# Performance work log

Hardware: AMD Instinct MI355X
Metric: run time of the kernel (lower is better)

Reference implementation:

```python
import jax, jax.numpy as jnp
import numpy as np

# Dimensions chosen per init_kwargs / input_specs
B, INC, OUTC, H, W = 16, 512, 256, 32, 32
FD = H * W           # flattened_dim = 1024 (perfect square)
DK = INC // 4        # 128, projection dim of the rotatory attention
EPS_BN = 1e-5


def setup_inputs() -> dict:
    key = jax.random.key(0)
    ks = jax.random.split(key, 8)
    sc = lambda fan_in: 1.0 / np.sqrt(fan_in)
    return {
        "x": jax.random.normal(ks[0], (B, INC, H, W), jnp.float32),
        "s": jax.random.normal(ks[1], (B, OUTC, 2 * H, 2 * W), jnp.float32),
        # ConvTranspose2d(inc, outc, 2, 2): torch weight shape (in, out, kH, kW)
        "up_w": jax.random.normal(ks[2], (INC, OUTC, 2, 2), jnp.float32) * sc(INC * 4),
        "up_b": jnp.zeros((OUTC,), jnp.float32),
        # LinearRotatoryAttentionModule projections: Linear(flattened_dim, inc//4) x3
        "wq": jax.random.normal(ks[3], (FD, DK), jnp.float32) * sc(FD),
        "wkl": jax.random.normal(ks[4], (FD, DK), jnp.float32) * sc(FD),
        "wkr": jax.random.normal(ks[5], (FD, DK), jnp.float32) * sc(FD),
        # conv_block(2*outc, outc): Conv2d 3x3 pad 1 + BatchNorm + ReLU
        "c1_w": jax.random.normal(ks[6], (OUTC, 2 * OUTC, 3, 3), jnp.float32) * sc(2 * OUTC * 9),
        "c1_b": jnp.zeros((OUTC,), jnp.float32),
        "bn_g": jnp.ones((OUTC,), jnp.float32),
        "bn_b": jnp.zeros((OUTC,), jnp.float32),
    }


def _rotatory(l, x, r, wq, wkl, wkr):
    """Linear rotatory attention on one triplet of slices, each (INC, FD).
    Center queries left and right contexts via elu+1 linear attention."""
    phi = lambda t: jax.nn.elu(t) + 1.0
    q = phi(x @ wq)        # (N, Dk)
    kl = phi(l @ wkl)      # (N, Dk)
    kr = phi(r @ wkr)      # (N, Dk)

    def linattn(k, v):
        kv = jnp.einsum('nk,nd->kd', k, v)      # (Dk, D)
        z = q @ k.sum(0) + 1e-6                  # (N,)
        return (q @ kv) / z[:, None]             # (N, D)

    return x + linattn(kl, l) + linattn(kr, r)


def reference(x, s, up_w, up_b, wq, wkl, wkr, c1_w, c1_b, bn_g, bn_b):
    # --- rotatory attention over interior batch samples (vectorized, no Python loop) ---
    xf = x.reshape(B, INC, FD)
    mid = jax.vmap(_rotatory, in_axes=(0, 0, 0, None, None, None))(
        xf[:-2], xf[1:-1], xf[2:], wq, wkl, wkr)          # (B-2, INC, FD)
    new = jnp.concatenate([x[:1], mid.reshape(B - 2, INC, H, W), x[-1:]], axis=0)

    # --- ConvTranspose2d k=2 s=2: non-overlapping, exact as einsum + reshape ---
    up = jnp.einsum('ncij,coab->noiajb', new, up_w).reshape(B, OUTC, 2 * H, 2 * W)
    up = up + up_b[None, :, None, None]

    # --- fused gate: sigmoid(relu(up + s)), then channel concat with skip ---
    g = jax.nn.sigmoid(jax.nn.relu(up + s))
    cat = jnp.concatenate([g, s], axis=1)                  # (B, 2*OUTC, 2H, 2W)

    # --- conv_block: Conv 3x3 same + BatchNorm (batch stats) + ReLU ---
    y = jax.lax.conv_general_dilated(cat, c1_w, (1, 1), 'SAME',
                                     dimension_numbers=('NCHW', 'OIHW', 'NCHW'))
    y = y + c1_b[None, :, None, None]
    mu = y.mean(axis=(0, 2, 3), keepdims=True)
    var = y.var(axis=(0, 2, 3), keepdims=True)
    y = (y - mu) / jnp.sqrt(var + EPS_BN)
    y = y * bn_g[None, :, None, None] + bn_b[None, :, None, None]
    return jax.nn.relu(y)
```

## Files before the change

### kernel.cpp

```cpp
#include <hip/hip_runtime.h>
#include <math.h>

#define B_ 16
#define INC 512
#define OUTC 256
#define FD 1024
#define DK 128
#define T_ 14
#define HO 64
#define WO 64
#define SP (HO*WO)
#define KCP 40

typedef unsigned short u16;
typedef __attribute__((ext_vector_type(8))) short shortx8;
typedef __attribute__((ext_vector_type(4))) float floatx4;

__device__ __forceinline__ float phi_f(float t) {
    return t > 0.0f ? t + 1.0f : expf(t);
}
__device__ __forceinline__ u16 f2bf(float f) {
    unsigned int u = __float_as_uint(f);
    unsigned int r = (u + 0x7fffu + ((u >> 16) & 1u)) >> 16;
    return (u16)r;
}
__device__ __forceinline__ float bf2f(u16 h) {
    return __uint_as_float(((unsigned int)h) << 16);
}

__global__ __launch_bounds__(256) void kprep_x(const float* __restrict__ x, u16* __restrict__ xT) {
    __shared__ u16 T[64][65];
    int d0 = blockIdx.x * 64, c0 = blockIdx.y * 64, b = blockIdx.z;
    const float* src = x + (size_t)b * INC * FD;
    int tid = threadIdx.x, lr = tid >> 6, lc = tid & 63;
    #pragma unroll
    for (int i = 0; i < 16; ++i) {
        int c = lr + i * 4;
        T[lc][c] = f2bf(src[(size_t)(c0 + c) * FD + d0 + lc]);
    }
    __syncthreads();
    u16* dst = xT + (size_t)b * FD * INC;
    #pragma unroll
    for (int i = 0; i < 16; ++i) {
        int d = lr + i * 4;
        dst[(size_t)(d0 + d) * INC + c0 + lc] = T[d][lc];
    }
}

__global__ __launch_bounds__(256) void ktr_w(const float* __restrict__ src, u16* __restrict__ dst,
                                             int R, int C) {
    __shared__ u16 T[64][65];
    int c0 = blockIdx.x * 64, r0 = blockIdx.y * 64;
    int tid = threadIdx.x, lr = tid >> 6, lc = tid & 63;
    #pragma unroll
    for (int i = 0; i < 16; ++i) {
        int r = lr + i * 4;
        T[lc][r] = f2bf(src[(size_t)(r0 + r) * C + c0 + lc]);
    }
    __syncthreads();
    #pragma unroll
    for (int i = 0; i < 16; ++i) {
        int c = lr + i * 4;
        dst[(size_t)(c0 + c) * R + r0 + lc] = T[c][lc];
    }
}

__global__ void kw_tr(const float* __restrict__ c1_w, u16* __restrict__ Wt) {
    int i = blockIdx.x * 256 + threadIdx.x;
    if (i >= 256 * 512 * 9) return;
    int tap = i % 9; int t2 = i / 9;
    int c = t2 % 512; int o = t2 / 512;
    Wt[((size_t)tap * 256 + o) * 512 + c] = f2bf(c1_w[i]);
}

__global__ __launch_bounds__(256) void k1_proj(const float* __restrict__ x,
        const u16* __restrict__ wqT, const u16* __restrict__ wklT, const u16* __restrict__ wkrT,
        u16* __restrict__ qb, u16* __restrict__ klt, u16* __restrict__ krt) {
    __shared__ u16 smem[8704];
    u16* As = smem;
    u16* Bs = smem + 5120;
    int z = blockIdx.z, t = z / 3, which = z - t * 3;
    int src = (which == 0) ? t + 1 : (which == 1 ? t : t + 2);
    const float* Af = x + (size_t)src * INC * FD;
    const u16* Bw = (which == 0) ? wqT : (which == 1 ? wklT : wkrT);
    int n0 = blockIdx.x * 64, m0 = blockIdx.y * 128;
    int tid = threadIdx.x, w = tid >> 6, lane = tid & 63, l15 = lane & 15, quad = lane >> 4;
    int sm = tid >> 2, sq = (tid & 3) * 8;
    floatx4 acc[2][4];
    #pragma unroll
    for (int i = 0; i < 2; ++i)
        #pragma unroll
        for (int j = 0; j < 4; ++j) acc[i][j] = (floatx4){0.f,0.f,0.f,0.f};

    for (int k0 = 0; k0 < FD; k0 += 32) {
        float4 v0 = *(const float4*)&Af[(size_t)(m0 + sm) * FD + k0 + sq];
        float4 v1 = *(const float4*)&Af[(size_t)(m0 + sm) * FD + k0 + sq + 4];
        float4 v2 = *(const float4*)&Af[(size_t)(m0 + 64 + sm) * FD + k0 + sq];
        float4 v3 = *(const float4*)&Af[(size_t)(m0 + 64 + sm) * FD + k0 + sq + 4];
        union { u16 h[8]; uint4 v; } p0, p1;
        p0.h[0]=f2bf(v0.x); p0.h[1]=f2bf(v0.y); p0.h[2]=f2bf(v0.z); p0.h[3]=f2bf(v0.w);
        p0.h[4]=f2bf(v1.x); p0.h[5]=f2bf(v1.y); p0.h[6]=f2bf(v1.z); p0.h[7]=f2bf(v1.w);
        p1.h[0]=f2bf(v2.x); p1.h[1]=f2bf(v2.y); p1.h[2]=f2bf(v2.z); p1.h[3]=f2bf(v2.w);
        p1.h[4]=f2bf(v3.x); p1.h[5]=f2bf(v3.y); p1.h[6]=f2bf(v3.z); p1.h[7]=f2bf(v3.w);
        *(uint4*)&As[sm * 40 + sq] = p0.v;
        *(uint4*)&As[(64 + sm) * 40 + sq] = p1.v;
        *(uint4*)&Bs[sm * 40 + sq] = *(const uint4*)&Bw[(size_t)(n0 + sm) * FD + k0 + sq];
        __syncthreads();
        shortx8 bfr[4];
        #pragma unroll
        for (int nt = 0; nt < 4; ++nt)
            bfr[nt] = *(const shortx8*)&Bs[(nt * 16 + l15) * 40 + quad * 8];
        #pragma unroll
        for (int mt = 0; mt < 2; ++mt) {
            shortx8 af = *(const shortx8*)&As[(w * 32 + mt * 16 + l15) * 40 + quad * 8];
            #pragma unroll
            for (int nt = 0; nt < 4; ++nt)
                acc[mt][nt] = __builtin_amdgcn_mfma_f32_16x16x32_bf16(af, bfr[nt], acc[mt][nt], 0, 0, 0);
        }
        __syncthreads();
    }
    if (which == 0) {
        u16* outp = qb + (size_t)t * INC * DK;
        #pragma unroll
        for (int mt = 0; mt < 2; ++mt)
            #pragma unroll
            for (int nt = 0; nt < 4; ++nt)
                #pragma unroll
                for (int r = 0; r < 4; ++r) {
                    int m_out = m0 + w * 32 + mt * 16 + quad * 4 + r;
                    int n_out = n0 + nt * 16 + l15;
                    outp[(size_t)m_out * DK + n_out] = f2bf(phi_f(acc[mt][nt][r]));
                }
    } else {
        u16* outp = ((which == 1) ? klt : krt) + (size_t)t * DK * INC;
        #pragma unroll
        for (int mt = 0; mt < 2; ++mt)
            #pragma unroll
            for (int nt = 0; nt < 4; ++nt)
                #pragma unroll
                for (int r = 0; r < 4; ++r) {
                    int mloc = w * 32 + mt * 16 + quad * 4 + r;
                    int nloc = nt * 16 + l15;
                    smem[nloc * 136 + mloc] = f2bf(phi_f(acc[mt][nt][r]));
                }
        __syncthreads();
        int dkl = tid >> 2, seg = tid & 3;
        const uint4* sp = (const uint4*)&smem[dkl * 136 + seg * 32];
        uint4* dp = (uint4*)&outp[(size_t)(n0 + dkl) * INC + m0 + seg * 32];
        dp[0] = sp[0]; dp[1] = sp[1]; dp[2] = sp[2]; dp[3] = sp[3];
    }
}

__global__ void k2b_ksum(const u16* __restrict__ klt, const u16* __restrict__ krt,
                         float* __restrict__ ksuml, float* __restrict__ ksumr) {
    int t = blockIdx.x; int dk = threadIdx.x;
    const u16* pl = klt + ((size_t)t * DK + dk) * INC;
    const u16* pr = krt + ((size_t)t * DK + dk) * INC;
    float s1 = 0.f, s2 = 0.f;
    for (int n = 0; n < INC; ++n) { s1 += bf2f(pl[n]); s2 += bf2f(pr[n]); }
    ksuml[t * DK + dk] = s1; ksumr[t * DK + dk] = s2;
}

__global__ void k2c_z(const u16* __restrict__ qb, const float* __restrict__ ksuml,
                      const float* __restrict__ ksumr, float* __restrict__ zl, float* __restrict__ zr) {
    int t = blockIdx.x; int n = threadIdx.x;
    const u16* q = qb + ((size_t)t * INC + n) * DK;
    const float* sl = ksuml + t * DK;
    const float* sr = ksumr + t * DK;
    float a = 0.f, b = 0.f;
    for (int k = 0; k < DK; ++k) { float qv = bf2f(q[k]); a = fmaf(qv, sl[k], a); b = fmaf(qv, sr[k], b); }
    zl[t * INC + n] = a + 1e-6f;
    zr[t * INC + n] = b + 1e-6f;
}

__global__ __launch_bounds__(256) void k2_kv(const u16* __restrict__ xT,
        const u16* __restrict__ klt, const u16* __restrict__ krt,
        u16* __restrict__ kvlT, u16* __restrict__ kvrT) {
    __shared__ u16 As[128 * 40];
    __shared__ u16 Bs[64 * 40];
    int z = blockIdx.z, t = z >> 1, side = z & 1;
    const u16* A = xT + (size_t)(side ? t + 2 : t) * FD * INC;
    const u16* Bw = (side ? krt : klt) + (size_t)t * DK * INC;
    u16* outp = (side ? kvrT : kvlT) + (size_t)t * FD * DK;
    int n0 = blockIdx.x * 64, m0 = blockIdx.y * 128;
    int tid = threadIdx.x, w = tid >> 6, lane = tid & 63, l15 = lane & 15, quad = lane >> 4;
    int sm = tid >> 2, sq = (tid & 3) * 8;
    floatx4 acc[2][4];
    #pragma unroll
    for (int i = 0; i < 2; ++i)
        #pragma unroll
        for (int j = 0; j < 4; ++j) acc[i][j] = (floatx4){0.f,0.f,0.f,0.f};
    for (int k0 = 0; k0 < INC; k0 += 32) {
        *(uint4*)&As[sm * 40 + sq] = *(const uint4*)&A[(size_t)(m0 + sm) * INC + k0 + sq];
        *(uint4*)&As[(64 + sm) * 40 + sq] = *(const uint4*)&A[(size_t)(m0 + 64 + sm) * INC + k0 + sq];
        *(uint4*)&Bs[sm * 40 + sq] = *(const uint4*)&Bw[(size_t)(n0 + sm) * INC + k0 + sq];
        __syncthreads();
        shortx8 bfr[4];
        #pragma unroll
        for (int nt = 0; nt < 4; ++nt)
            bfr[nt] = *(const shortx8*)&Bs[(nt * 16 + l15) * 40 + quad * 8];
        #pragma unroll
        for (int mt = 0; mt < 2; ++mt) {
            shortx8 af = *(const shortx8*)&As[(w * 32 + mt * 16 + l15) * 40 + quad * 8];
            #pragma unroll
            for (int nt = 0; nt < 4; ++nt)
                acc[mt][nt] = __builtin_amdgcn_mfma_f32_16x16x32_bf16(af, bfr[nt], acc[mt][nt], 0, 0, 0);
        }
        __syncthreads();
    }
    #pragma unroll
    for (int mt = 0; mt < 2; ++mt)
        #pragma unroll
        for (int nt = 0; nt < 4; ++nt)
            #pragma unroll
            for (int r = 0; r < 4; ++r) {
                int m_out = m0 + w * 32 + mt * 16 + quad * 4 + r;
                int n_out = n0 + nt * 16 + l15;
                outp[(size_t)m_out * DK + n_out] = f2bf(acc[mt][nt][r]);
            }
}

__global__ __launch_bounds__(256) void k3_out(const u16* __restrict__ xT,
        const u16* __restrict__ qb, const u16* __restrict__ kvlT, const u16* __restrict__ kvrT,
        const float* __restrict__ zl, const float* __restrict__ zr, u16* __restrict__ newT) {
    __shared__ u16 As1[128 * 40];
    __shared__ u16 As2[128 * 40];
    __shared__ u16 Bs[64 * 40];
    int t = blockIdx.z;
    const u16* A1 = kvlT + (size_t)t * FD * DK;
    const u16* A2 = kvrT + (size_t)t * FD * DK;
    const u16* Bq = qb + (size_t)t * INC * DK;
    int n0 = blockIdx.x * 64, m0 = blockIdx.y * 128;
    int tid = threadIdx.x, w = tid >> 6, lane = tid & 63, l15 = lane & 15, quad = lane >> 4;
    int sm = tid >> 2, sq = (tid & 3) * 8;
    floatx4 accl[2][4], accr[2][4];
    #pragma unroll
    for (int i = 0; i < 2; ++i)
        #pragma unroll
        for (int j = 0; j < 4; ++j) {
            accl[i][j] = (floatx4){0.f,0.f,0.f,0.f};
            accr[i][j] = (floatx4){0.f,0.f,0.f,0.f};
        }
    for (int k0 = 0; k0 < DK; k0 += 32) {
        *(uint4*)&As1[sm * 40 + sq] = *(const uint4*)&A1[(size_t)(m0 + sm) * DK + k0 + sq];
        *(uint4*)&As1[(64 + sm) * 40 + sq] = *(const uint4*)&A1[(size_t)(m0 + 64 + sm) * DK + k0 + sq];
        *(uint4*)&As2[sm * 40 + sq] = *(const uint4*)&A2[(size_t)(m0 + sm) * DK + k0 + sq];
        *(uint4*)&As2[(64 + sm) * 40 + sq] = *(const uint4*)&A2[(size_t)(m0 + 64 + sm) * DK + k0 + sq];
        *(uint4*)&Bs[sm * 40 + sq] = *(const uint4*)&Bq[(size_t)(n0 + sm) * DK + k0 + sq];
        __syncthreads();
        shortx8 bfr[4];
        #pragma unroll
        for (int nt = 0; nt < 4; ++nt)
            bfr[nt] = *(const shortx8*)&Bs[(nt * 16 + l15) * 40 + quad * 8];
        #pragma unroll
        for (int mt = 0; mt < 2; ++mt) {
            shortx8 afl = *(const shortx8*)&As1[(w * 32 + mt * 16 + l15) * 40 + quad * 8];
            shortx8 afr = *(const shortx8*)&As2[(w * 32 + mt * 16 + l15) * 40 + quad * 8];
            #pragma unroll
            for (int nt = 0; nt < 4; ++nt) {
                accl[mt][nt] = __builtin_amdgcn_mfma_f32_16x16x32_bf16(afl, bfr[nt], accl[mt][nt], 0, 0, 0);
                accr[mt][nt] = __builtin_amdgcn_mfma_f32_16x16x32_bf16(afr, bfr[nt], accr[mt][nt], 0, 0, 0);
            }
        }
        __syncthreads();
    }
    float il[4], ir[4];
    #pragma unroll
    for (int nt = 0; nt < 4; ++nt) {
        int n_out = n0 + nt * 16 + l15;
        il[nt] = 1.0f / zl[t * INC + n_out];
        ir[nt] = 1.0f / zr[t * INC + n_out];
    }
    const u16* xc = xT + (size_t)(t + 1) * FD * INC;
    u16* outp = newT + (size_t)t * FD * INC;
    #pragma unroll
    for (int mt = 0; mt < 2; ++mt)
        #pragma unroll
        for (int nt = 0; nt < 4; ++nt)
            #pragma unroll
            for (int r = 0; r < 4; ++r) {
                int m_out = m0 + w * 32 + mt * 16 + quad * 4 + r;
                int n_out = n0 + nt * 16 + l15;
                float xv = bf2f(xc[(size_t)m_out * INC + n_out]);
                float v = xv + accl[mt][nt][r] * il[nt] + accr[mt][nt][r] * ir[nt];
                outp[(size_t)m_out * INC + n_out] = f2bf(v);
            }
}

__global__ __launch_bounds__(256) void k4_up(const u16* __restrict__ xT,
        const u16* __restrict__ newT, const u16* __restrict__ upwT,
        const float* __restrict__ up_b, u16* __restrict__ P) {
    __shared__ u16 As[128 * 40];
    __shared__ u16 Bs[64 * 40];
    int b = blockIdx.z;
    const u16* A = (b == 0) ? xT
                 : (b == B_ - 1) ? (xT + (size_t)(B_ - 1) * FD * INC)
                 : (newT + (size_t)(b - 1) * FD * INC);
    int n0 = blockIdx.x * 64, m0 = blockIdx.y * 128;
    int tid = threadIdx.x, w = tid >> 6, lane = tid & 63, l15 = lane & 15, quad = lane >> 4;
    int sm = tid >> 2, sq = (tid & 3) * 8;
    floatx4 acc[2][4];
    #pragma unroll
    for (int i = 0; i < 2; ++i)
        #pragma unroll
        for (int j = 0; j < 4; ++j) acc[i][j] = (floatx4){0.f,0.f,0.f,0.f};
    for (int k0 = 0; k0 < INC; k0 += 32) {
        *(uint4*)&As[sm * 40 + sq] = *(const uint4*)&A[(size_t)(m0 + sm) * INC + k0 + sq];
        *(uint4*)&As[(64 + sm) * 40 + sq] = *(const uint4*)&A[(size_t)(m0 + 64 + sm) * INC + k0 + sq];
        *(uint4*)&Bs[sm * 40 + sq] = *(const uint4*)&upwT[(size_t)(n0 + sm) * INC + k0 + sq];
        __syncthreads();
        shortx8 bfr[4];
        #pragma unroll
        for (int nt = 0; nt < 4; ++nt)
            bfr[nt] = *(const shortx8*)&Bs[(nt * 16 + l15) * 40 + quad * 8];
        #pragma unroll
        for (int mt = 0; mt < 2; ++mt) {
            shortx8 af = *(const shortx8*)&As[(w * 32 + mt * 16 + l15) * 40 + quad * 8];
            #pragma unroll
            for (int nt = 0; nt < 4; ++nt)
                acc[mt][nt] = __builtin_amdgcn_mfma_f32_16x16x32_bf16(af, bfr[nt], acc[mt][nt], 0, 0, 0);
        }
        __syncthreads();
    }
    #pragma unroll
    for (int mt = 0; mt < 2; ++mt)
        #pragma unroll
        for (int nt = 0; nt < 4; ++nt) {
            int mm = n0 + nt * 16 + l15;
            int o = mm >> 2, aa = (mm >> 1) & 1, cb = mm & 1;
            float bias = up_b[o];
            #pragma unroll
            for (int r = 0; r < 4; ++r) {
                int px = m0 + w * 32 + mt * 16 + quad * 4 + r;
                int ii = px >> 5, jj = px & 31;
                int p = 2 * ii + aa, q = 2 * jj + cb;
                size_t pos = ((size_t)(b * 66 + 1 + p) * 66 + 1 + q) * 512;
                float sv = bf2f(P[pos + 256 + o]);
                float up = acc[mt][nt][r] + bias;
                float rr = fmaxf(up + sv, 0.0f);
                P[pos + o] = f2bf(1.0f / (1.0f + expf(-rr)));
            }
        }
}

__global__ __launch_bounds__(256) void k4b_sfill(const float* __restrict__ s_in,
                                                 u16* __restrict__ P) {
    __shared__ u16 T[64 * 264];
    int p = blockIdx.x;
    int b = blockIdx.y;
    int tid = threadIdx.x;
    int qcol = tid & 63;
    int ob = tid >> 6;
    for (int o = ob; o < 256; o += 4) {
        float v = s_in[((size_t)(b * OUTC + o) * HO + p) * WO + qcol];
        T[qcol * 264 + o] = f2bf(v);
    }
    __syncthreads();
    int q2 = tid >> 2;
    int sg = tid & 3;
    size_t base = ((size_t)(b * 66 + 1 + p) * 66 + 1 + q2) * 512 + 256;
    #pragma unroll
    for (int it = 0; it < 8; ++it) {
        int seg = sg + it * 4;
        uint4 v = *(const uint4*)&T[q2 * 264 + seg * 8];
        *(uint4*)(P + base + seg * 8) = v;
    }
}

__global__ __launch_bounds__(256) void k5_mfma(const u16* __restrict__ P,
        const u16* __restrict__ Wt, const float* __restrict__ c1_b,
        float* __restrict__ y) {
    __shared__ u16 Xs[6 * 66 * KCP];
    int rb = blockIdx.x;
    int o0 = blockIdx.y * 64;
    int b  = blockIdx.z;
    int tid = threadIdx.x;
    int w = tid >> 6, lane = tid & 63;
    int l15 = lane & 15, quad = lane >> 4;

    floatx4 acc[4][4];
    #pragma unroll
    for (int i = 0; i < 4; ++i)
        #pragma unroll
        for (int j = 0; j < 4; ++j)
            acc[i][j] = (floatx4){0.f, 0.f, 0.f, 0.f};

    size_t Pbase = ((size_t)b * 66 + (size_t)rb * 4) * 66 * 512;

    for (int ch = 0; ch < 16; ++ch) {
        int c0 = ch * 32;
        __syncthreads();
        for (int s = tid; s < 1584; s += 256) {
            int r = s / 264; int rem = s - r * 264;
            int col = rem >> 2; int cs = rem & 3;
            uint4 v = *(const uint4*)(P + Pbase + ((size_t)r * 66 + col) * 512 + c0 + cs * 8);
            *(uint4*)&Xs[(r * 66 + col) * KCP + cs * 8] = v;
        }
        __syncthreads();
        #pragma unroll
        for (int dy = 0; dy < 3; ++dy) {
            #pragma unroll
            for (int dx = 0; dx < 3; ++dx) {
                int tap = dy * 3 + dx;
                shortx8 wf[4];
                #pragma unroll
                for (int nt = 0; nt < 4; ++nt)
                    wf[nt] = *(const shortx8*)(Wt +
                        ((size_t)(tap * 256 + o0 + nt * 16 + l15)) * 512 + c0 + quad * 8);
                #pragma unroll
                for (int mt = 0; mt < 4; ++mt) {
                    shortx8 af = *(const shortx8*)&Xs[((w + dy) * 66 + mt * 16 + l15 + dx) * KCP + quad * 8];
                    #pragma unroll
                    for (int nt = 0; nt < 4; ++nt)
                        acc[mt][nt] = __builtin_amdgcn_mfma_f32_16x16x32_bf16(
                            af, wf[nt], acc[mt][nt], 0, 0, 0);
                }
            }
        }
    }
    int row = rb * 4 + w;
    float bias[4];
    #pragma unroll
    for (int nt = 0; nt < 4; ++nt) bias[nt] = c1_b[o0 + nt * 16 + l15];
    #pragma unroll
    for (int mt = 0; mt < 4; ++mt) {
        #pragma unroll
        for (int nt = 0; nt < 4; ++nt) {
            int o = o0 + nt * 16 + l15;
            size_t ybase = (size_t)(b * OUTC + o) * SP + row * 64;
            #pragma unroll
            for (int r = 0; r < 4; ++r) {
                int col = mt * 16 + quad * 4 + r;
                y[ybase + col] = acc[mt][nt][r] + bias[nt];
            }
        }
    }
}

__global__ __launch_bounds__(256) void k6_bnred(const float* __restrict__ y,
        float* __restrict__ bnsum, float* __restrict__ bnsq) {
    int b = blockIdx.x, o = blockIdx.y;
    const float* p = y + ((size_t)b * OUTC + o) * SP;
    float s1 = 0.f, s2 = 0.f;
    for (int i = threadIdx.x; i < SP; i += 256) { float v = p[i]; s1 += v; s2 = fmaf(v, v, s2); }
    #pragma unroll
    for (int off = 32; off > 0; off >>= 1) {
        s1 += __shfl_down(s1, off, 64);
        s2 += __shfl_down(s2, off, 64);
    }
    __shared__ float r1[4], r2[4];
    int wid = threadIdx.x >> 6, lane = threadIdx.x & 63;
    if (lane == 0) { r1[wid] = s1; r2[wid] = s2; }
    __syncthreads();
    if (threadIdx.x == 0) {
        atomicAdd(&bnsum[o], r1[0] + r1[1] + r1[2] + r1[3]);
        atomicAdd(&bnsq[o],  r2[0] + r2[1] + r2[2] + r2[3]);
    }
}

__global__ void k7_bnfin(const float* __restrict__ bnsum, const float* __restrict__ bnsq,
                         const float* __restrict__ bn_g, const float* __restrict__ bn_b,
                         float* __restrict__ scale, float* __restrict__ shift) {
    int o = threadIdx.x;
    float cnt = (float)(B_ * SP);
    float mu = bnsum[o] / cnt;
    float var = bnsq[o] / cnt - mu * mu;
    float sc = bn_g[o] * rsqrtf(var + 1e-5f);
    scale[o] = sc;
    shift[o] = bn_b[o] - mu * sc;
}

__global__ __launch_bounds__(256) void k8_apply(float* __restrict__ y,
        const float* __restrict__ scale, const float* __restrict__ shift) {
    int i = blockIdx.x * 256 + threadIdx.x;
    int o = (i >> 10) & 255;
    float4 v = ((float4*)y)[i];
    float sc = scale[o], sh = shift[o];
    v.x = fmaxf(fmaf(v.x, sc, sh), 0.f);
    v.y = fmaxf(fmaf(v.y, sc, sh), 0.f);
    v.z = fmaxf(fmaf(v.z, sc, sh), 0.f);
    v.w = fmaxf(fmaf(v.w, sc, sh), 0.f);
    ((float4*)y)[i] = v;
}

extern "C" void kernel_launch(void* const* d_in, const int* in_sizes, int n_in,
                              void* d_out, int out_size, void* d_ws, size_t ws_size,
                              hipStream_t stream) {
    const float* x    = (const float*)d_in[0];
    const float* s_in = (const float*)d_in[1];
    const float* up_w = (const float*)d_in[2];
    const float* up_b = (const float*)d_in[3];
    const float* wq   = (const float*)d_in[4];
    const float* wkl  = (const float*)d_in[5];
    const float* wkr  = (const float*)d_in[6];
    const float* c1_w = (const float*)d_in[7];
    const float* c1_b = (const float*)d_in[8];
    const float* bn_g = (const float*)d_in[9];
    const float* bn_b = (const float*)d_in[10];
    float* y = (float*)d_out;
    float* ws = (float*)d_ws;

    size_t off = 0;
    float* ksuml = ws + off; off += (size_t)T_ * DK;
    float* ksumr = ws + off; off += (size_t)T_ * DK;
    float* zl    = ws + off; off += (size_t)T_ * INC;
    float* zr    = ws + off; off += (size_t)T_ * INC;
    float* bnsum = ws + off; off += OUTC;
    float* bnsq  = ws + off; off += OUTC;
    float* scale = ws + off; off += OUTC;
    float* shift = ws + off; off += OUTC;

    u16* ub = (u16*)(ws + off);
    size_t uo = 0;
    u16* qb   = ub + uo; uo += (size_t)T_ * INC * DK;
    u16* klt  = ub + uo; uo += (size_t)T_ * DK * INC;
    u16* krt  = ub + uo; uo += (size_t)T_ * DK * INC;
    u16* kvlT = ub + uo; uo += (size_t)T_ * FD * DK;
    u16* kvrT = ub + uo; uo += (size_t)T_ * FD * DK;
    u16* newT = ub + uo; uo += (size_t)T_ * FD * INC;
    u16* xT   = ub + uo; uo += (size_t)B_ * FD * INC;
    u16* wqT  = ub + uo; uo += (size_t)DK * FD;
    u16* wklT = ub + uo; uo += (size_t)DK * FD;
    u16* wkrT = ub + uo; uo += (size_t)DK * FD;
    u16* upwT = ub + uo; uo += (size_t)FD * INC;
    u16* Wt   = ub + uo; uo += (size_t)9 * OUTC * 2 * INC;
    u16* P    = ub + uo; uo += (size_t)B_ * 66 * 66 * 512;

    hipMemsetAsync(bnsum, 0, 2 * OUTC * sizeof(float), stream);
    hipMemsetAsync(P, 0, (size_t)B_ * 66 * 66 * 512 * sizeof(u16), stream);

    kprep_x<<<dim3(16, 8, B_), dim3(256), 0, stream>>>(x, xT);
    ktr_w<<<dim3(2, 16), dim3(256), 0, stream>>>(wq, wqT, FD, DK);
    ktr_w<<<dim3(2, 16), dim3(256), 0, stream>>>(wkl, wklT, FD, DK);
    ktr_w<<<dim3(2, 16), dim3(256), 0, stream>>>(wkr, wkrT, FD, DK);
    ktr_w<<<dim3(16, 8), dim3(256), 0, stream>>>(up_w, upwT, INC, FD);
    kw_tr<<<dim3((256 * 512 * 9 + 255) / 256), dim3(256), 0, stream>>>(c1_w, Wt);

    k1_proj<<<dim3(2, 4, 42), dim3(256), 0, stream>>>(x, wqT, wklT, wkrT, qb, klt, krt);
    k2b_ksum<<<dim3(T_), dim3(DK), 0, stream>>>(klt, krt, ksuml, ksumr);
    k2c_z<<<dim3(T_), dim3(INC), 0, stream>>>(qb, ksuml, ksumr, zl, zr);
    k2_kv<<<dim3(2, 8, 28), dim3(256), 0, stream>>>(xT, klt, krt, kvlT, kvrT);
    k3_out<<<dim3(8, 8, T_), dim3(256), 0, stream>>>(xT, qb, kvlT, kvrT, zl, zr, newT);
    k4b_sfill<<<dim3(64, B_), dim3(256), 0, stream>>>(s_in, P);
    k4_up<<<dim3(16, 8, B_), dim3(256), 0, stream>>>(xT, newT, upwT, up_b, P);
    k5_mfma<<<dim3(16, 4, B_), dim3(256), 0, stream>>>(P, Wt, c1_b, y);
    k6_bnred<<<dim3(B_, OUTC), dim3(256), 0, stream>>>(y, bnsum, bnsq);
    k7_bnfin<<<dim3(1), dim3(OUTC), 0, stream>>>(bnsum, bnsq, bn_g, bn_b, scale, shift);
    k8_apply<<<dim3((B_ * OUTC * SP / 4) / 256), dim3(256), 0, stream>>>(y, scale, shift);
}
```

Measured before the change: 708.9 us.

## Zero only padding border, stage k4_up epilogue through LDS, use direct global-to-LDS loads in conv

Replaces the full memset of the padded conv input buffer with a small kernel that zeroes only the border pixels. k4_up now transposes its accumulator tile through shared memory so the gate epilogue reads the skip channels and writes results with 16-byte vector accesses instead of scattered 2-byte ones. k5_mfma stages its input tile with global_load_lds into an unpadded 32-wide LDS layout, skipping the register round trip. The risk is bank conflicts from dropping the LDS row padding, and a correctness dependence on the LDS destination layout matching the lane ordering.

```diff
diff --git a/kernel.cpp b/kernel.cpp
--- a/kernel.cpp
+++ b/kernel.cpp
@@ -10,7 +10,7 @@
 #define HO 64
 #define WO 64
 #define SP (HO*WO)
-#define KCP 40
+#define KC5 32
 
 typedef unsigned short u16;
 typedef __attribute__((ext_vector_type(8))) short shortx8;
@@ -71,6 +71,22 @@
     int tap = i % 9; int t2 = i / 9;
     int c = t2 % 512; int o = t2 / 512;
     Wt[((size_t)tap * 256 + o) * 512 + c] = f2bf(c1_w[i]);
+}
+
+__global__ __launch_bounds__(256) void kborder(u16* __restrict__ P) {
+    int b = blockIdx.y;
+    int cbase = blockIdx.x * 20;
+    uint4 z = {0, 0, 0, 0};
+    for (int i = threadIdx.x; i < 20 * 64; i += 256) {
+        int c = cbase + (i >> 6);
+        int sub = i & 63;
+        int row, col;
+        if (c < 66)       { row = 0;       col = c; }
+        else if (c < 132) { row = 65;      col = c - 66; }
+        else if (c < 196) { row = c - 131; col = 0; }
+        else              { row = c - 195; col = 65; }
+        *(uint4*)(P + ((size_t)(b * 66 + row) * 66 + col) * 512 + sub * 8) = z;
+    }
 }
 
 __global__ __launch_bounds__(256) void k1_proj(const float* __restrict__ x,
@@ -290,8 +306,9 @@
 __global__ __launch_bounds__(256) void k4_up(const u16* __restrict__ xT,
         const u16* __restrict__ newT, const u16* __restrict__ upwT,
         const float* __restrict__ up_b, u16* __restrict__ P) {
-    __shared__ u16 As[128 * 40];
-    __shared__ u16 Bs[64 * 40];
+    __shared__ u16 smem[12288];
+    u16* As = smem;
+    u16* Bs = smem + 5120;
     int b = blockIdx.z;
     const u16* A = (b == 0) ? xT
                  : (b == B_ - 1) ? (xT + (size_t)(B_ - 1) * FD * INC)
@@ -322,25 +339,45 @@
         }
         __syncthreads();
     }
+    u16* Ts = smem;
+    int ppos = (l15 & 3) * 128;
     #pragma unroll
     for (int mt = 0; mt < 2; ++mt)
         #pragma unroll
         for (int nt = 0; nt < 4; ++nt) {
-            int mm = n0 + nt * 16 + l15;
-            int o = mm >> 2, aa = (mm >> 1) & 1, cb = mm & 1;
-            float bias = up_b[o];
+            int lm = nt * 16 + l15;
+            float bias = up_b[(n0 + lm) >> 2];
+            int o_rel = lm >> 2;
             #pragma unroll
             for (int r = 0; r < 4; ++r) {
-                int px = m0 + w * 32 + mt * 16 + quad * 4 + r;
-                int ii = px >> 5, jj = px & 31;
-                int p = 2 * ii + aa, q = 2 * jj + cb;
-                size_t pos = ((size_t)(b * 66 + 1 + p) * 66 + 1 + q) * 512;
-                float sv = bf2f(P[pos + 256 + o]);
-                float up = acc[mt][nt][r] + bias;
-                float rr = fmaxf(up + sv, 0.0f);
-                P[pos + o] = f2bf(1.0f / (1.0f + expf(-rr)));
-            }
-        }
+                int l = w * 32 + mt * 16 + quad * 4 + r;
+                Ts[(ppos + l) * 24 + o_rel] = f2bf(acc[mt][nt][r] + bias);
+            }
+        }
+    __syncthreads();
+    #pragma unroll
+    for (int j2 = 0; j2 < 2; ++j2) {
+        int pi = tid + j2 * 256;
+        int pp = pi >> 7, l = pi & 127;
+        int aa = pp >> 1, cbb = pp & 1;
+        int px = m0 + l;
+        int row = 2 * (px >> 5) + aa, colq = 2 * (px & 31) + cbb;
+        size_t dst = ((size_t)(b * 66 + 1 + row) * 66 + 1 + colq) * 512 + (n0 >> 2);
+        union { uint4 v; u16 h[8]; } a0, a1, s0, s1, g0, g1;
+        a0.v = *(const uint4*)&Ts[pi * 24];
+        a1.v = *(const uint4*)&Ts[pi * 24 + 8];
+        s0.v = *(const uint4*)(P + dst + 256);
+        s1.v = *(const uint4*)(P + dst + 256 + 8);
+        #pragma unroll
+        for (int e = 0; e < 8; ++e) {
+            float r0 = fmaxf(bf2f(a0.h[e]) + bf2f(s0.h[e]), 0.0f);
+            float r1 = fmaxf(bf2f(a1.h[e]) + bf2f(s1.h[e]), 0.0f);
+            g0.h[e] = f2bf(1.0f / (1.0f + expf(-r0)));
+            g1.h[e] = f2bf(1.0f / (1.0f + expf(-r1)));
+        }
+        *(uint4*)(P + dst) = g0.v;
+        *(uint4*)(P + dst + 8) = g1.v;
+    }
 }
 
 __global__ __launch_bounds__(256) void k4b_sfill(const float* __restrict__ s_in,
@@ -370,7 +407,7 @@
 __global__ __launch_bounds__(256) void k5_mfma(const u16* __restrict__ P,
         const u16* __restrict__ Wt, const float* __restrict__ c1_b,
         float* __restrict__ y) {
-    __shared__ u16 Xs[6 * 66 * KCP];
+    __shared__ u16 Xs[6 * 66 * KC5];
     int rb = blockIdx.x;
     int o0 = blockIdx.y * 64;
     int b  = blockIdx.z;
@@ -390,11 +427,18 @@
     for (int ch = 0; ch < 16; ++ch) {
         int c0 = ch * 32;
         __syncthreads();
-        for (int s = tid; s < 1584; s += 256) {
-            int r = s / 264; int rem = s - r * 264;
-            int col = rem >> 2; int cs = rem & 3;
-            uint4 v = *(const uint4*)(P + Pbase + ((size_t)r * 66 + col) * 512 + c0 + cs * 8);
-            *(uint4*)&Xs[(r * 66 + col) * KCP + cs * 8] = v;
+        #pragma unroll
+        for (int it = 0; it < 7; ++it) {
+            int s = it * 256 + tid;
+            if (s < 1584) {
+                int r = s / 264, rem = s - r * 264;
+                int col = rem >> 2, cs = rem & 3;
+                const u16* gp = P + Pbase + ((size_t)r * 66 + col) * 512 + c0 + cs * 8;
+                __builtin_amdgcn_global_load_lds(
+                    (const __attribute__((address_space(1))) void*)gp,
+                    (__attribute__((address_space(3))) void*)&Xs[(size_t)(it * 256 + w * 64) * 8],
+                    16, 0, 0);
+            }
         }
         __syncthreads();
         #pragma unroll
@@ -409,7 +453,7 @@
                         ((size_t)(tap * 256 + o0 + nt * 16 + l15)) * 512 + c0 + quad * 8);
                 #pragma unroll
                 for (int mt = 0; mt < 4; ++mt) {
-                    shortx8 af = *(const shortx8*)&Xs[((w + dy) * 66 + mt * 16 + l15 + dx) * KCP + quad * 8];
+                    shortx8 af = *(const shortx8*)&Xs[((w + dy) * 66 + mt * 16 + l15 + dx) * KC5 + quad * 8];
                     #pragma unroll
                     for (int nt = 0; nt < 4; ++nt)
                         acc[mt][nt] = __builtin_amdgcn_mfma_f32_16x16x32_bf16(
@@ -527,8 +571,8 @@
     u16* P    = ub + uo; uo += (size_t)B_ * 66 * 66 * 512;
 
     hipMemsetAsync(bnsum, 0, 2 * OUTC * sizeof(float), stream);
-    hipMemsetAsync(P, 0, (size_t)B_ * 66 * 66 * 512 * sizeof(u16), stream);
-
+
+    kborder<<<dim3(13, B_), dim3(256), 0, stream>>>(P);
     kprep_x<<<dim3(16, 8, B_), dim3(256), 0, stream>>>(x, xT);
     ktr_w<<<dim3(2, 16), dim3(256), 0, stream>>>(wq, wqT, FD, DK);
     ktr_w<<<dim3(2, 16), dim3(256), 0, stream>>>(wkl, wklT, FD, DK);
```

After: 687.6 us. 1.03x faster.
